# Performance work log

Measured on AMD Instinct MI355X. Metric: run time of the kernel, lower is better.

Reference implementation:

```python
import jax, jax.numpy as jnp
import numpy as np

N_WIRES = 8
DIM = 2 ** N_WIRES  # 256
N_OPS = 20

# Fixed realization of tq.RandomLayer(n_ops=20): ops drawn once with a fixed seed.
_rs = np.random.RandomState(0)
RAND_OPS = []
for _ in range(N_OPS):
    k = int(_rs.randint(4))
    if k == 3:
        c, t = _rs.choice(N_WIRES, 2, replace=False)
        RAND_OPS.append(("cnot", int(c), int(t)))
    else:
        RAND_OPS.append((("rx", "ry", "rz")[k], int(_rs.randint(N_WIRES)), 0))

_idx = np.arange(DIM)
# Z eigenvalue sign per wire per basis state (wire 0 = most significant bit)
ZSIGN_NP = np.stack([1.0 - 2.0 * ((_idx >> (N_WIRES - 1 - w)) & 1) for w in range(N_WIRES)]).astype(np.float32)
ZSIGN = jnp.asarray(ZSIGN_NP)        # [8, 256]
ZS_T = jnp.asarray(ZSIGN_NP.T)       # [256, 8]

# CNOT is a basis permutation: precompute index maps for each cnot op.
PERMS = {}
for _i, _op in enumerate(RAND_OPS):
    if _op[0] == "cnot":
        _c, _t = _op[1], _op[2]
        _cb = (_idx >> (N_WIRES - 1 - _c)) & 1
        PERMS[_i] = jnp.asarray(_idx ^ (_cb << (N_WIRES - 1 - _t)))


def _ry_mat(t):
    c = jnp.cos(t * 0.5).astype(jnp.complex64)
    s = jnp.sin(t * 0.5).astype(jnp.complex64)
    return jnp.stack([jnp.stack([c, -s]), jnp.stack([s, c])])


def _rx_mat(t):
    c = jnp.cos(t * 0.5).astype(jnp.complex64)
    s = (-1j * jnp.sin(t * 0.5)).astype(jnp.complex64)
    return jnp.stack([jnp.stack([c, s]), jnp.stack([s, c])])


def _apply_1q(state, U, w):
    # state: [B, 256]; apply 2x2 U on wire w
    B = state.shape[0]
    s = state.reshape(B, 2 ** w, 2, -1)
    return jnp.einsum('ij,bajc->baic', U, s).reshape(B, DIM)


def _forward(x, ry_theta, rand_params, W1, b1, W2, b2):
    B, S, E = x.shape
    f = x.reshape(B * S, E)[:, :N_WIRES]  # encoder uses input_idx 0..7
    # Encoder: RY(f_w) on |0> for each wire -> product state, built by kron chain
    c = jnp.cos(f * 0.5)
    s = jnp.sin(f * 0.5)
    state = jnp.ones((B * S, 1), jnp.float32)
    for w in range(N_WIRES):
        v = jnp.stack([c[:, w], s[:, w]], axis=-1)  # [BS, 2]
        state = (state[:, :, None] * v[:, None, :]).reshape(B * S, -1)
    state = state.astype(jnp.complex64)  # [BS, 256]
    # Fixed random layer
    for i, op in enumerate(RAND_OPS):
        kind = op[0]
        if kind == "cnot":
            state = state[:, PERMS[i]]
        elif kind == "rz":
            ph = jnp.exp((-0.5j * rand_params[i]) * ZSIGN[op[1]]).astype(jnp.complex64)
            state = state * ph[None, :]
        elif kind == "rx":
            state = _apply_1q(state, _rx_mat(rand_params[i]), op[1])
        else:
            state = _apply_1q(state, _ry_mat(rand_params[i]), op[1])
    # Trainable per-wire RY gates
    for w in range(N_WIRES):
        state = _apply_1q(state, _ry_mat(ry_theta[w]), w)
    # MeasureAll(PauliZ): <Z_w> = sum_b |amp_b|^2 * zsign_w(b)
    probs = (state.real ** 2 + state.imag ** 2)  # [BS, 256] float32
    expv = probs @ ZS_T                          # [BS, 8]
    h = jax.nn.relu(expv @ W1.T + b1)
    out = h @ W2.T + b2
    return out.reshape(B, S, -1)


def setup_inputs() -> dict:
    key = jax.random.key(0)
    k1, k2, k3, k4, k5 = jax.random.split(key, 5)
    B, S, E = 4, 4096, 512
    pi = 3.14159265
    x = jax.random.normal(k1, (B, S, E), jnp.float32)
    ry_theta = jax.random.uniform(k2, (N_WIRES,), jnp.float32, -pi, pi)
    rand_params = jax.random.uniform(k3, (N_OPS,), jnp.float32, -pi, pi)
    W1 = jax.random.normal(k4, (64, N_WIRES), jnp.float32) * (1.0 / np.sqrt(N_WIRES))
    b1 = jnp.zeros((64,), jnp.float32)
    W2 = jax.random.normal(k5, (E, 64), jnp.float32) * (1.0 / 8.0)
    b2 = jnp.zeros((E,), jnp.float32)
    return {"x": x, "ry_theta": ry_theta, "rand_params": rand_params, "W1": W1, "b1": b1, "W2": W2, "b2": b2}


def reference(x, ry_theta, rand_params, W1, b1, W2, b2):
    return _forward(x, ry_theta, rand_params, W1, b1, W2, b2)
```

## Files before the change

### kernel.cpp

```cpp
#include <hip/hip_runtime.h>
#include <hip/hip_fp16.h>
#include <cstdint>

#define N_RAND   20
#define N_GATES  28
#define E_DIM    512
#define TPB_TILES 4

struct OpsArg { int d[N_GATES]; };

struct MT19937ce {
  uint32_t mt[624] = {};
  int mti = 0;
  constexpr void seed(uint32_t s){
    mt[0]=s;
    for(int i=1;i<624;i++) mt[i]=1812433253u*(mt[i-1]^(mt[i-1]>>30))+(uint32_t)i;
    mti=624;
  }
  constexpr uint32_t next(){
    if(mti>=624){
      for(int i=0;i<624;i++){
        uint32_t y=(mt[i]&0x80000000u)|(mt[(i+1)%624]&0x7fffffffu);
        mt[i]=mt[(i+397)%624]^(y>>1)^((y&1u)?0x9908b0dfu:0u);
      }
      mti=0;
    }
    uint32_t y=mt[mti++];
    y^=y>>11; y^=(y<<7)&0x9d2c5680u; y^=(y<<15)&0xefc60000u; y^=y>>18;
    return y;
  }
  constexpr uint32_t interval(uint32_t mx){
    if(!mx) return 0;
    uint32_t mask=mx; mask|=mask>>1; mask|=mask>>2; mask|=mask>>4; mask|=mask>>8; mask|=mask>>16;
    uint32_t v = next()&mask;
    while(v>mx) v = next()&mask;
    return v;
  }
};

constexpr OpsArg build_ops_ce(){
  MT19937ce rs; rs.seed(0);
  OpsArg o{};
  for(int i=0;i<N_RAND;i++){
    uint32_t k = rs.interval(3);
    if(k==3){
      int perm[8] = {0,1,2,3,4,5,6,7};
      for(int j=7;j>=1;j--){
        uint32_t t=rs.interval((uint32_t)j);
        int tmp=perm[j]; perm[j]=perm[t]; perm[t]=tmp;
      }
      o.d[i] = 3 | (perm[0]<<2) | (perm[1]<<5);
    } else {
      uint32_t w = rs.interval(7);
      o.d[i] = (int)k | ((int)w<<2);
    }
  }
  for(int i=0;i<8;i++) o.d[N_RAND+i] = 1 | (i<<2);
  return o;
}
inline constexpr OpsArg OPS = build_ops_ce();

__device__ __forceinline__ float readlane_f(float v, int l){
  return __int_as_float(__builtin_amdgcn_readlane(__float_as_int(v), l));
}
template<int CTRL>
__device__ __forceinline__ float dpp_mov(float v){
  int s = __float_as_int(v);
  return __int_as_float(__builtin_amdgcn_update_dpp(s, s, CTRL, 0xF, 0xF, false));
}
template<int M>
__device__ __forceinline__ float xl(float v){
  if constexpr (M==1)      return dpp_mov<0xB1>(v);
  else if constexpr (M==2) return dpp_mov<0x4E>(v);
  else return __int_as_float(__builtin_amdgcn_ds_swizzle(__float_as_int(v), (M<<10)|0x1F));
}
template<int L>
__device__ __forceinline__ float bcast(float v){
  return __int_as_float(__builtin_amdgcn_ds_swizzle(__float_as_int(v), L<<5));
}

typedef _Float16 v2h __attribute__((ext_vector_type(2)));
typedef _Float16 v8h __attribute__((ext_vector_type(8)));
typedef float    v4f __attribute__((ext_vector_type(4)));
union HU  { uint32_t u; v2h h; };

template<int G>
__device__ __forceinline__ void run_gates(float (&ar)[8], float (&ai)[8],
                                          const float (&sgn)[5], int l,
                                          float cv, float sv)
{
  if constexpr (G < N_GATES){
    constexpr int dd   = OPS.d[G];
    constexpr int kind = dd & 3;
    constexpr int wa   = (dd>>2) & 7;
    constexpr int wb   = (dd>>5) & 7;
    const float gc = readlane_f(cv, G);
    const float gs = readlane_f(sv, G);

    if constexpr (kind == 3){
      if constexpr (wa < 3 && wb < 3){
        constexpr int Rc = 4>>wa, Rt = 4>>wb;
        #pragma unroll
        for (int r=0;r<8;r++){
          if ((r & Rc) && !(r & Rt)){
            float t0=ar[r]; ar[r]=ar[r|Rt]; ar[r|Rt]=t0;
            float t1=ai[r]; ai[r]=ai[r|Rt]; ai[r|Rt]=t1;
          }
        }
      } else if constexpr (wa < 3){
        constexpr int Rc = 4>>wa, Mt = 16>>(wb-3);
        #pragma unroll
        for (int r=0;r<8;r++){
          if (r & Rc){ ar[r]=xl<Mt>(ar[r]); ai[r]=xl<Mt>(ai[r]); }
        }
      } else if constexpr (wb < 3){
        constexpr int Mc = 16>>(wa-3), Rt = 4>>wb;
        const bool cb = (l & Mc) != 0;
        #pragma unroll
        for (int r=0;r<8;r++){
          if (!(r & Rt)){
            float alo=ar[r], ahi=ar[r|Rt];
            ar[r]    = cb ? ahi : alo;  ar[r|Rt] = cb ? alo : ahi;
            float blo=ai[r], bhi=ai[r|Rt];
            ai[r]    = cb ? bhi : blo;  ai[r|Rt] = cb ? blo : bhi;
          }
        }
      } else {
        constexpr int Mc = 16>>(wa-3), Mt = 16>>(wb-3);
        const bool cb = (l & Mc) != 0;
        #pragma unroll
        for (int r=0;r<8;r++){
          float pr = xl<Mt>(ar[r]), pi_ = xl<Mt>(ai[r]);
          ar[r] = cb ? pr  : ar[r];
          ai[r] = cb ? pi_ : ai[r];
        }
      }
    } else if constexpr (kind == 2){
      if constexpr (wa < 3){
        constexpr int Rb = 4>>wa;
        #pragma unroll
        for (int r=0;r<8;r++){
          const float pim = (r & Rb) ? gs : -gs;
          float nr = gc*ar[r] - pim*ai[r];
          ai[r] = gc*ai[r] + pim*ar[r];
          ar[r] = nr;
        }
      } else {
        constexpr int SI = wa-3;
        const float pim = sgn[SI]*gs;
        #pragma unroll
        for (int r=0;r<8;r++){
          float nr = gc*ar[r] - pim*ai[r];
          ai[r] = gc*ai[r] + pim*ar[r];
          ar[r] = nr;
        }
      }
    } else if constexpr (kind == 1){
      if constexpr (wa < 3){
        constexpr int Rb = 4>>wa;
        #pragma unroll
        for (int r=0;r<8;r++){
          if (!(r & Rb)){
            const int h = r|Rb;
            float lr=ar[r], li=ai[r], hr=ar[h], hii=ai[h];
            ar[r]=gc*lr - gs*hr;  ai[r]=gc*li - gs*hii;
            ar[h]=gs*lr + gc*hr;  ai[h]=gs*li + gc*hii;
          }
        }
      } else {
        constexpr int M = 16>>(wa-3), SI = wa-3;
        const float sg = sgn[SI]*gs;
        #pragma unroll
        for (int r=0;r<8;r++){
          float pr = xl<M>(ar[r]), pi_ = xl<M>(ai[r]);
          ar[r] = gc*ar[r] + sg*pr;
          ai[r] = gc*ai[r] + sg*pi_;
        }
      }
    } else {
      if constexpr (wa < 3){
        constexpr int Rb = 4>>wa;
        #pragma unroll
        for (int r=0;r<8;r++){
          if (!(r & Rb)){
            const int h = r|Rb;
            float lr=ar[r], li=ai[r], hr=ar[h], hii=ai[h];
            ar[r]=gc*lr + gs*hii;  ai[r]=gc*li - gs*hr;
            ar[h]=gc*hr + gs*li;   ai[h]=gc*hii - gs*lr;
          }
        }
      } else {
        constexpr int M = 16>>(wa-3);
        #pragma unroll
        for (int r=0;r<8;r++){
          float pr = xl<M>(ar[r]), pi_ = xl<M>(ai[r]);
          ar[r] = gc*ar[r] + gs*pi_;
          ai[r] = gc*ai[r] - gs*pr;
        }
      }
    }
    run_gates<G+1>(ar, ai, sgn, l, cv, sv);
  }
}

__global__ __launch_bounds__(512)
void qffb_pre(const float* __restrict__ ry_theta,
              const float* __restrict__ rand_params,
              _Float16* __restrict__ Urf,
              _Float16* __restrict__ Uif)
{
  const int tid  = threadIdx.x;
  const int lane = tid & 63;
  const int l    = lane & 31;
  const int wave = tid >> 6;
  const int b    = blockIdx.x*16 + wave*2 + (lane>>5);

  float th = 0.f;
  if (lane < N_GATES)
    th = (lane < N_RAND) ? rand_params[lane] : ry_theta[lane - N_RAND];
  float cv, sv;
  __sincosf(0.5f*th, &sv, &cv);

  float sgn[5];
  sgn[0] = (l&16) ? 1.f : -1.f;
  sgn[1] = (l& 8) ? 1.f : -1.f;
  sgn[2] = (l& 4) ? 1.f : -1.f;
  sgn[3] = (l& 2) ? 1.f : -1.f;
  sgn[4] = (l& 1) ? 1.f : -1.f;

  float ar[8], ai[8];
  #pragma unroll
  for (int r=0;r<8;r++){
    ar[r] = (((b>>5)==r) && ((b&31)==l)) ? 1.f : 0.f;
    ai[r] = 0.f;
  }

  run_gates<0>(ar, ai, sgn, l, cv, sv);

  const int k  = b >> 5;
  const int qd = (b >> 3) & 3;
  const int jj = b & 7;
  #pragma unroll
  for (int r=0;r<8;r++){
    const int j   = r*32 + l;
    const int nt  = j >> 4;
    const int rr_ = j & 15;
    const size_t F = ((size_t)((nt*8 + k)*4 + qd)*16 + rr_)*8 + jj;
    Urf[F] = (_Float16)ar[r];
    Uif[F] = (_Float16)ai[r];
  }
}

#define PSTRIDE 272
#define PFSTR   264
__global__ __launch_bounds__(512)
void qffb_main(const float* __restrict__ x,
               const _Float16* __restrict__ Urf,
               const _Float16* __restrict__ Uif,
               const float* __restrict__ W1,
               const float* __restrict__ b1,
               const float* __restrict__ W2,
               const float* __restrict__ b2,
               float* __restrict__ out)
{
  __shared__ _Float16 Ps[16*PSTRIDE];
  __shared__ _Float16 Hs[16][72];
  __shared__ float    Ts[8][16*68];
  float* Pf = &Ts[0][0];

  const int tid  = threadIdx.x;
  const int lane = tid & 63;
  const int l    = lane & 31;
  const int wave = tid >> 6;
  const int rr   = lane & 15;
  const int quad = lane >> 4;
  const int trow = wave*2 + (lane>>5);

  const size_t ub0 = ((size_t)((wave*2+0)*32 + quad)*16 + rr)*8;
  const size_t ub1 = ((size_t)((wave*2+1)*32 + quad)*16 + rr)*8;
  v8h Br0[8], Bi0[8], Br1[8], Bi1[8];
  #pragma unroll
  for (int k=0;k<8;++k){
    const size_t o = (size_t)k*512;
    Br0[k] = *(const v8h*)(Urf + ub0 + o);
    Bi0[k] = *(const v8h*)(Uif + ub0 + o);
    Br1[k] = *(const v8h*)(Urf + ub1 + o);
    Bi1[k] = *(const v8h*)(Uif + ub1 + o);
  }

  float sgn[5];
  sgn[0] = (l&16) ? 1.f : -1.f;
  sgn[1] = (l& 8) ? 1.f : -1.f;
  sgn[2] = (l& 4) ? 1.f : -1.f;
  sgn[3] = (l& 2) ? 1.f : -1.f;
  sgn[4] = (l& 1) ? 1.f : -1.f;

  const float4 wA0 = *(const float4*)(W1 + (size_t)(2*l)*8);
  const float4 wA1 = *(const float4*)(W1 + (size_t)(2*l)*8 + 4);
  const float4 wB0 = *(const float4*)(W1 + (size_t)(2*l+1)*8);
  const float4 wB1 = *(const float4*)(W1 + (size_t)(2*l+1)*8 + 4);
  const float2 bb  = *(const float2*)(b1 + 2*l);

  const int ng = wave;
  v8h WB0[4], WB1[4];
  #pragma unroll
  for (int j=0;j<4;++j){
    const int e = ng*64 + j*16 + rr;
    const float4 wa = *(const float4*)(W2 + (size_t)e*64 + quad*8);
    const float4 wb = *(const float4*)(W2 + (size_t)e*64 + quad*8 + 4);
    const float4 wc = *(const float4*)(W2 + (size_t)e*64 + 32 + quad*8);
    const float4 wd = *(const float4*)(W2 + (size_t)e*64 + 32 + quad*8 + 4);
    WB0[j] = v8h{(_Float16)wa.x,(_Float16)wa.y,(_Float16)wa.z,(_Float16)wa.w,
                 (_Float16)wb.x,(_Float16)wb.y,(_Float16)wb.z,(_Float16)wb.w};
    WB1[j] = v8h{(_Float16)wc.x,(_Float16)wc.y,(_Float16)wc.z,(_Float16)wc.w,
                 (_Float16)wd.x,(_Float16)wd.y,(_Float16)wd.z,(_Float16)wd.w};
  }
  const float4 bias = *(const float4*)(b2 + ng*64 + rr*4);

  for (int it=0; it<TPB_TILES; ++it){
    const int tileIdx = blockIdx.x*TPB_TILES + it;
    const int token   = tileIdx*16 + trow;

    {
      const float4 xa = *(const float4*)(x + (size_t)token*E_DIM);
      const float4 xb = *(const float4*)(x + (size_t)token*E_DIM + 4);
      float c[8], s[8];
      float xs[8] = {xa.x, xa.y, xa.z, xa.w, xb.x, xb.y, xb.z, xb.w};
      #pragma unroll
      for (int w=0; w<8; ++w) __sincosf(0.5f*xs[w], &s[w], &c[w]);
      float L = ((l&16)? s[0]:c[0]) * ((l&8)? s[1]:c[1]);
      L *= ((l&4)? s[2]:c[2]) * ((l&2)? s[3]:c[3]);
      L *= ((l&1)? s[4]:c[4]);
      const float p67[4] = {c[6]*c[7], c[6]*s[7], s[6]*c[7], s[6]*s[7]};
      v8h v;
      #pragma unroll
      for (int i=0;i<8;++i)
        v[i] = (_Float16)(L * (((i&4)? s[5]:c[5]) * p67[i&3]));
      *(v8h*)&Ps[trow*PSTRIDE + l*8] = v;
    }
    __syncthreads();

    v4f accr[2], acci[2];
    #pragma unroll
    for (int n=0;n<2;++n){ accr[n]=v4f{0.f,0.f,0.f,0.f}; acci[n]=v4f{0.f,0.f,0.f,0.f}; }

    #pragma unroll
    for (int k=0;k<8;++k){
      const v8h a0 = *(const v8h*)&Ps[rr*PSTRIDE + k*32 + quad*8];
      accr[0] = __builtin_amdgcn_mfma_f32_16x16x32_f16(a0, Br0[k], accr[0], 0,0,0);
      acci[0] = __builtin_amdgcn_mfma_f32_16x16x32_f16(a0, Bi0[k], acci[0], 0,0,0);
      accr[1] = __builtin_amdgcn_mfma_f32_16x16x32_f16(a0, Br1[k], accr[1], 0,0,0);
      acci[1] = __builtin_amdgcn_mfma_f32_16x16x32_f16(a0, Bi1[k], acci[1], 0,0,0);
    }

    #pragma unroll
    for (int n=0;n<2;++n){
      const int nt = wave*2 + n;
      #pragma unroll
      for (int r2=0;r2<4;++r2)
        Pf[(quad*4+r2)*PFSTR + nt*16 + rr] =
            accr[n][r2]*accr[n][r2] + acci[n][r2]*acci[n][r2];
    }
    __syncthreads();

    {
      float p[8];
      #pragma unroll
      for (int r=0;r<8;r++) p[r] = Pf[trow*PFSTR + r*32 + l];

      const float t1a=p[0]+p[1], t1b=p[2]+p[3], t1c=p[4]+p[5], t1d=p[6]+p[7];
      const float s0a=t1a+t1b, s0b=t1c+t1d;
      float P  = s0a + s0b;
      float e0 = s0a - s0b;
      float e1 = (t1a+t1c) - (t1b+t1d);
      float e2 = (p[0]-p[1])+(p[2]-p[3])+(p[4]-p[5])+(p[6]-p[7]);
      {
        float t;
        t=xl<1>(e0); e0+=t;  t=xl<1>(e1); e1+=t;  t=xl<1>(e2); e2+=t;
        t=xl<1>(P);  P = fmaf(-sgn[4], P, t);
        t=xl<2>(e0); e0+=t;  t=xl<2>(e1); e1+=t;  t=xl<2>(e2); e2+=t;
        t=xl<2>(P);  P = fmaf(-sgn[3], P, t);
        t=xl<4>(e0); e0+=t;  t=xl<4>(e1); e1+=t;  t=xl<4>(e2); e2+=t;
        t=xl<4>(P);  P = fmaf(-sgn[2], P, t);
        t=xl<8>(e0); e0+=t;  t=xl<8>(e1); e1+=t;  t=xl<8>(e2); e2+=t;
        t=xl<8>(P);  P = fmaf(-sgn[1], P, t);
        t=xl<16>(e0); e0+=t; t=xl<16>(e1); e1+=t; t=xl<16>(e2); e2+=t;
        t=xl<16>(P); P = fmaf(-sgn[0], P, t);
      }
      const float e3 = bcast<16>(P);
      const float e4 = bcast<8>(P);
      const float e5 = bcast<4>(P);
      const float e6 = bcast<2>(P);
      const float e7 = bcast<1>(P);

      float h0 = bb.x + wA0.x*e0 + wA0.y*e1 + wA0.z*e2 + wA0.w*e3
                      + wA1.x*e4 + wA1.y*e5 + wA1.z*e6 + wA1.w*e7;
      float h1 = bb.y + wB0.x*e0 + wB0.y*e1 + wB0.z*e2 + wB0.w*e3
                      + wB1.x*e4 + wB1.y*e5 + wB1.z*e6 + wB1.w*e7;
      HU pk;
      pk.h = v2h{(_Float16)fmaxf(h0,0.f), (_Float16)fmaxf(h1,0.f)};
      *(uint32_t*)((char*)&Hs[trow][0] + 4*l) = pk.u;
    }
    __syncthreads();

    {
      const v8h a0 = *(const v8h*)&Hs[rr][quad*8];
      const v8h a1 = *(const v8h*)&Hs[rr][32 + quad*8];

      #pragma unroll
      for (int j=0;j<4;++j){
        v4f acc = {0.f,0.f,0.f,0.f};
        acc = __builtin_amdgcn_mfma_f32_16x16x32_f16(a0, WB0[j], acc, 0, 0, 0);
        acc = __builtin_amdgcn_mfma_f32_16x16x32_f16(a1, WB1[j], acc, 0, 0, 0);
        #pragma unroll
        for (int r2=0;r2<4;r2++)
          Ts[wave][(quad*4+r2)*68 + j*16 + rr] = acc[r2];
      }

      #pragma unroll
      for (int k=0;k<4;++k){
        const int row = 4*k + quad;
        float4 v = *(const float4*)&Ts[wave][row*68 + rr*4];
        v.x += bias.x; v.y += bias.y; v.z += bias.z; v.w += bias.w;
        const int t = tileIdx*16 + row;
        *(float4*)(out + (size_t)t*E_DIM + ng*64 + rr*4) = v;
      }
    }
  }
}

extern "C" void kernel_launch(void* const* d_in, const int* in_sizes, int n_in,
                              void* d_out, int out_size, void* d_ws, size_t ws_size,
                              hipStream_t stream)
{
  (void)n_in; (void)out_size; (void)ws_size;
  const int ntok = in_sizes[0] / E_DIM;
  char* ws = (char*)d_ws;
  _Float16* Urf = (_Float16*)(ws);
  _Float16* Uif = (_Float16*)(ws + 131072);

  qffb_pre<<<16, 512, 0, stream>>>(
      (const float*)d_in[1],
      (const float*)d_in[2],
      Urf, Uif);

  qffb_main<<<ntok/16/TPB_TILES, 512, 0, stream>>>(
      (const float*)d_in[0],
      Urf, Uif,
      (const float*)d_in[3],
      (const float*)d_in[4],
      (const float*)d_in[5],
      (const float*)d_in[6],
      (float*)d_out);
}
```

Before: 109.3 us.

## Fold Z-sign measurement into W1 and compute hidden layer via MFMA

Precomputes a combined 256x64 fp16 matrix (ZSIGN^T · W1^T) in registers and replaces the shuffle-based PauliZ reduction plus scalar W1 matvec with an MFMA over fp16 probabilities stored in shared memory. Only four waves do this stage, which removes the per-lane DPP/swizzle butterfly work and the float probability buffer. In exchange, probabilities and the folded weights are rounded to fp16, which may cost accuracy, and the other waves sit idle during this stage.

Result: no change. 109.3 us (median of 2 runs) (+0.0%).

```diff
diff --git a/kernel.cpp b/kernel.cpp
--- a/kernel.cpp
+++ b/kernel.cpp
@@ -74,15 +74,10 @@
   else if constexpr (M==2) return dpp_mov<0x4E>(v);
   else return __int_as_float(__builtin_amdgcn_ds_swizzle(__float_as_int(v), (M<<10)|0x1F));
 }
-template<int L>
-__device__ __forceinline__ float bcast(float v){
-  return __int_as_float(__builtin_amdgcn_ds_swizzle(__float_as_int(v), L<<5));
-}
 
 typedef _Float16 v2h __attribute__((ext_vector_type(2)));
 typedef _Float16 v8h __attribute__((ext_vector_type(8)));
 typedef float    v4f __attribute__((ext_vector_type(4)));
-union HU  { uint32_t u; v2h h; };
 
 template<int G>
 __device__ __forceinline__ void run_gates(float (&ar)[8], float (&ai)[8],
@@ -252,7 +247,7 @@
 }
 
 #define PSTRIDE 272
-#define PFSTR   264
+#define PQSTR   264
 __global__ __launch_bounds__(512)
 void qffb_main(const float* __restrict__ x,
                const _Float16* __restrict__ Urf,
@@ -264,9 +259,9 @@
                float* __restrict__ out)
 {
   __shared__ _Float16 Ps[16*PSTRIDE];
+  __shared__ _Float16 Pq[16*PQSTR];
   __shared__ _Float16 Hs[16][72];
   __shared__ float    Ts[8][16*68];
-  float* Pf = &Ts[0][0];
 
   const int tid  = threadIdx.x;
   const int lane = tid & 63;
@@ -288,18 +283,29 @@
     Bi1[k] = *(const v8h*)(Uif + ub1 + o);
   }
 
-  float sgn[5];
-  sgn[0] = (l&16) ? 1.f : -1.f;
-  sgn[1] = (l& 8) ? 1.f : -1.f;
-  sgn[2] = (l& 4) ? 1.f : -1.f;
-  sgn[3] = (l& 2) ? 1.f : -1.f;
-  sgn[4] = (l& 1) ? 1.f : -1.f;
-
-  const float4 wA0 = *(const float4*)(W1 + (size_t)(2*l)*8);
-  const float4 wA1 = *(const float4*)(W1 + (size_t)(2*l)*8 + 4);
-  const float4 wB0 = *(const float4*)(W1 + (size_t)(2*l+1)*8);
-  const float4 wB1 = *(const float4*)(W1 + (size_t)(2*l+1)*8 + 4);
-  const float2 bb  = *(const float2*)(b1 + 2*l);
+  v8h WZ[8];
+  float b1o = 0.f;
+  if (wave < 4){
+    const int o = wave*16 + rr;
+    const float4 w1a = *(const float4*)(W1 + (size_t)o*8);
+    const float4 w1b = *(const float4*)(W1 + (size_t)o*8 + 4);
+    b1o = b1[o];
+    const float q = ((quad&2)? -w1a.w : w1a.w) + ((quad&1)? -w1b.x : w1b.x);
+    float sk[8], sj[8];
+    #pragma unroll
+    for (int k=0;k<8;++k)
+      sk[k] = ((k&4)? -w1a.x : w1a.x) + ((k&2)? -w1a.y : w1a.y) + ((k&1)? -w1a.z : w1a.z);
+    #pragma unroll
+    for (int jj=0;jj<8;++jj)
+      sj[jj] = ((jj&4)? -w1b.y : w1b.y) + ((jj&2)? -w1b.z : w1b.z) + ((jj&1)? -w1b.w : w1b.w);
+    #pragma unroll
+    for (int k=0;k<8;++k){
+      v8h t;
+      #pragma unroll
+      for (int jj=0;jj<8;++jj) t[jj] = (_Float16)(sk[k] + q + sj[jj]);
+      WZ[k] = t;
+    }
+  }
 
   const int ng = wave;
   v8h WB0[4], WB1[4];
@@ -357,49 +363,25 @@
     for (int n=0;n<2;++n){
       const int nt = wave*2 + n;
       #pragma unroll
-      for (int r2=0;r2<4;++r2)
-        Pf[(quad*4+r2)*PFSTR + nt*16 + rr] =
-            accr[n][r2]*accr[n][r2] + acci[n][r2]*acci[n][r2];
+      for (int r2=0;r2<4;++r2){
+        const float pv = accr[n][r2]*accr[n][r2] + acci[n][r2]*acci[n][r2];
+        Pq[(quad*4+r2)*PQSTR + nt*16 + rr] = (_Float16)pv;
+      }
     }
     __syncthreads();
 
-    {
-      float p[8];
-      #pragma unroll
-      for (int r=0;r<8;r++) p[r] = Pf[trow*PFSTR + r*32 + l];
-
-      const float t1a=p[0]+p[1], t1b=p[2]+p[3], t1c=p[4]+p[5], t1d=p[6]+p[7];
-      const float s0a=t1a+t1b, s0b=t1c+t1d;
-      float P  = s0a + s0b;
-      float e0 = s0a - s0b;
-      float e1 = (t1a+t1c) - (t1b+t1d);
-      float e2 = (p[0]-p[1])+(p[2]-p[3])+(p[4]-p[5])+(p[6]-p[7]);
-      {
-        float t;
-        t=xl<1>(e0); e0+=t;  t=xl<1>(e1); e1+=t;  t=xl<1>(e2); e2+=t;
-        t=xl<1>(P);  P = fmaf(-sgn[4], P, t);
-        t=xl<2>(e0); e0+=t;  t=xl<2>(e1); e1+=t;  t=xl<2>(e2); e2+=t;
-        t=xl<2>(P);  P = fmaf(-sgn[3], P, t);
-        t=xl<4>(e0); e0+=t;  t=xl<4>(e1); e1+=t;  t=xl<4>(e2); e2+=t;
-        t=xl<4>(P);  P = fmaf(-sgn[2], P, t);
-        t=xl<8>(e0); e0+=t;  t=xl<8>(e1); e1+=t;  t=xl<8>(e2); e2+=t;
-        t=xl<8>(P);  P = fmaf(-sgn[1], P, t);
-        t=xl<16>(e0); e0+=t; t=xl<16>(e1); e1+=t; t=xl<16>(e2); e2+=t;
-        t=xl<16>(P); P = fmaf(-sgn[0], P, t);
-      }
-      const float e3 = bcast<16>(P);
-      const float e4 = bcast<8>(P);
-      const float e5 = bcast<4>(P);
-      const float e6 = bcast<2>(P);
-      const float e7 = bcast<1>(P);
-
-      float h0 = bb.x + wA0.x*e0 + wA0.y*e1 + wA0.z*e2 + wA0.w*e3
-                      + wA1.x*e4 + wA1.y*e5 + wA1.z*e6 + wA1.w*e7;
-      float h1 = bb.y + wB0.x*e0 + wB0.y*e1 + wB0.z*e2 + wB0.w*e3
-                      + wB1.x*e4 + wB1.y*e5 + wB1.z*e6 + wB1.w*e7;
-      HU pk;
-      pk.h = v2h{(_Float16)fmaxf(h0,0.f), (_Float16)fmaxf(h1,0.f)};
-      *(uint32_t*)((char*)&Hs[trow][0] + 4*l) = pk.u;
+    if (wave < 4){
+      v4f acc = {0.f,0.f,0.f,0.f};
+      #pragma unroll
+      for (int k=0;k<8;++k){
+        const v8h a = *(const v8h*)&Pq[rr*PQSTR + k*32 + quad*8];
+        acc = __builtin_amdgcn_mfma_f32_16x16x32_f16(a, WZ[k], acc, 0,0,0);
+      }
+      #pragma unroll
+      for (int r2=0;r2<4;++r2){
+        const float h = fmaxf(acc[r2] + b1o, 0.f);
+        Hs[quad*4+r2][wave*16 + rr] = (_Float16)h;
+      }
     }
     __syncthreads();
 
```
